# Kernel optimization log

Measured on AMD Instinct MI355X. Metric: run time of the kernel, lower is better.

## Reference

```python
import jax, jax.numpy as jnp
import numpy as np

BS, C, H, W = 16, 192, 120, 120
AN = 36            # agent_num
KS = 3             # kernel_size
POOL = 6           # int(sqrt(agent_num))
MID = 2 * AN // 4  # 18
EPS = 1e-5


def _conv(x, w, groups=1):
    return jax.lax.conv_general_dilated(
        x, w, window_strides=(1, 1), padding='SAME',
        dimension_numbers=('NCHW', 'OIHW', 'NCHW'),
        feature_group_count=groups)


def _bn(x, g, b, m, v):
    # inference-mode BatchNorm2d with running stats
    inv = g / jnp.sqrt(v + EPS)
    return x * inv[None, :, None, None] + (b - m * inv)[None, :, None, None]


def _pool6(x):
    # AdaptiveAvgPool2d(6) with H,W divisible by 6 == exact average pooling
    bs, c, h, w = x.shape
    return x.reshape(bs, c, POOL, h // POOL, POOL, w // POOL).mean(axis=(3, 5))


def setup_inputs() -> dict:
    key = jax.random.key(0)
    ks = jax.random.split(key, 14)
    u = lambda k, s: jax.random.uniform(k, s, jnp.float32, 0.5, 1.5)
    n = lambda k, s, sc: jax.random.normal(k, s, jnp.float32) * sc
    return {
        'x':      n(ks[0], (BS, C, H, W), 1.0),
        'key_w':  n(ks[1], (C, C // 3, KS, KS), 0.05),   # grouped conv, groups=3
        'bn1_g':  u(ks[2], (C,)),
        'bn1_b':  n(ks[3], (C,), 0.1),
        'bn1_m':  n(ks[4], (C,), 0.1),
        'bn1_v':  u(ks[5], (C,)),
        'val_w':  n(ks[6], (C, C, 1, 1), 0.05),
        'att_w1': n(ks[7], (MID, 2 * AN, 1, 1), 0.1),
        'bn2_g':  u(ks[8], (MID,)),
        'bn2_b':  n(ks[9], (MID,), 0.1),
        'bn2_m':  n(ks[10], (MID,), 0.1),
        'bn2_v':  u(ks[11], (MID,)),
        'att_w2': n(ks[12], (KS * KS * AN, MID, 1, 1), 0.1),
        'att_b2': n(ks[13], (KS * KS * AN,), 0.1),
    }


def reference(x, key_w, bn1_g, bn1_b, bn1_m, bn1_v, val_w,
              att_w1, bn2_g, bn2_b, bn2_m, bn2_v, att_w2, att_b2):
    bs, c, h, w = x.shape
    hw = h * w
    # key embedding: grouped conv -> BN -> ReLU
    k1 = jax.nn.relu(_bn(_conv(x, key_w, groups=3), bn1_g, bn1_b, bn1_m, bn1_v))
    # agent tokens and pooled values (torch .view semantics: raw row-major reshape)
    agent = _pool6(x).reshape(bs, AN, c)                 # (bs, 36, c)  channel-mixed view
    v = _pool6(_conv(x, val_w)).reshape(bs, c, AN)       # (bs, c, 36)
    k1r = k1.reshape(bs, hw, c)                          # torch k1.view(bs,-1,c)
    q1 = x.reshape(bs, hw, c)
    # agent<->key and query<->agent attention
    agent_attn = jax.nn.softmax(jnp.einsum('bac,bnc->ban', agent, k1r), axis=-1)  # (bs,36,hw)
    q_attn = jax.nn.softmax(jnp.einsum('bnc,bac->bna', q1, agent), axis=-1)       # (bs,hw,36)
    y = jnp.concatenate([agent_attn, jnp.swapaxes(q_attn, 1, 2)], axis=1)          # (bs,72,hw)
    y = y.reshape(bs, 2 * AN, h, w)
    # conv-generated attention map
    t = jax.nn.relu(_bn(_conv(y, att_w1), bn2_g, bn2_b, bn2_m, bn2_v))
    att = _conv(t, att_w2) + att_b2[None, :, None, None]                           # (bs,324,h,w)
    att = att.reshape(bs, AN, KS * KS, h, w).mean(axis=2).reshape(bs, hw, AN)
    k2 = jax.nn.softmax(att, axis=-1)                                              # (bs,hw,36)
    k2v = jnp.einsum('bna,bca->bnc', k2, v)                                        # (bs,hw,c)
    out = jnp.swapaxes(k2v, 1, 2).reshape(bs, c, h, w) + k1
    return out
```

## Files before the change

kernel.cpp:

```cpp
#include <hip/hip_runtime.h>
#include <hip/hip_bf16.h>
#include <math.h>

#define BS 16
#define C 192
#define H 120
#define W 120
#define HW 14400
#define AN 36
#define MID 18
#define CPG 64
#define EPS 1e-5f
#define SPX 128
#define BPS 200
#define NWQ 13824
#define XROWS 122
#define XCOLS 132
#define OPX 64
#define WST 72

typedef __attribute__((ext_vector_type(8))) short s16x8;
typedef __attribute__((ext_vector_type(4))) float f32x4;
typedef __attribute__((ext_vector_type(4))) unsigned short u16x4;

static __device__ __forceinline__ short f2bf(float f) {
    union { float f; unsigned u; } v; v.f = f;
    unsigned r = (v.u + 0x7FFF + ((v.u >> 16) & 1)) >> 16;
    return (short)r;
}
static __device__ __forceinline__ float bf2f(unsigned short u) {
    union { unsigned u; float f; } v; v.u = ((unsigned)u) << 16;
    return v.f;
}
static __device__ __forceinline__ s16x8 cvt8(float4 f0, float4 f1) {
    s16x8 v;
    v[0] = f2bf(f0.x); v[1] = f2bf(f0.y); v[2] = f2bf(f0.z); v[3] = f2bf(f0.w);
    v[4] = f2bf(f1.x); v[5] = f2bf(f1.y); v[6] = f2bf(f1.z); v[7] = f2bf(f1.w);
    return v;
}

__global__ __launch_bounds__(256) void k_wfold(const float* __restrict__ kw,
                                               const float* __restrict__ g1,
                                               const float* __restrict__ v1,
                                               unsigned short* __restrict__ Wq) {
    int u = blockIdx.x * 256 + threadIdx.x;
    if (u >= NWQ) return;
    int gc = u / 2304, rem = u - gc * 2304;
    int g = gc >> 1, cc = gc & 1;
    int th = rem >> 6, co = rem & 63;
    int tap = th >> 2, hi = th & 3;
    int cog = g * 64 + co;
    float inv = g1[cog] * rsqrtf(v1[cog] + EPS);
    const float* wp = kw + ((size_t)cog * 64 + cc * 32 + hi * 8) * 9 + tap;
    s16x8 v;
    #pragma unroll
    for (int e = 0; e < 8; ++e) v[e] = f2bf(wp[e * 9] * inv);
    *(s16x8*)&Wq[(size_t)u * 8] = v;
}

__global__ __launch_bounds__(256) void k_xt(const float* __restrict__ x,
                                            unsigned short* __restrict__ xTp) {
    int y = blockIdx.x, b = blockIdx.y;
    int t = threadIdx.x;
    __shared__ unsigned short L[120 * 200];
    for (int u = t; u < 24 * 120; u += 256) {
        int oc = u / 120, px = u - oc * 120;
        const float* xp = x + ((size_t)b * C + oc * 8) * HW + y * W + px;
        s16x8 v;
        #pragma unroll
        for (int j = 0; j < 8; ++j) v[j] = f2bf(xp[(size_t)j * HW]);
        *(s16x8*)&L[px * 200 + oc * 8] = v;
    }
    __syncthreads();
    for (int u = t; u < 24 * XCOLS; u += 256) {
        int oc = u / XCOLS, p = u - oc * XCOLS;
        int px = p - 1;
        s16x8 v = {0, 0, 0, 0, 0, 0, 0, 0};
        if (px >= 0 && px < 120) v = *(const s16x8*)&L[px * 200 + oc * 8];
        *(s16x8*)&xTp[(((size_t)(b * 24 + oc)) * XROWS + (y + 1)) * XCOLS * 8 + p * 8] = v;
    }
    if (y == 0 || y == H - 1) {
        int r = (y == 0) ? 0 : XROWS - 1;
        s16x8 z = {0, 0, 0, 0, 0, 0, 0, 0};
        for (int u = t; u < 24 * XCOLS; u += 256) {
            int oc = u / XCOLS, p = u - oc * XCOLS;
            *(s16x8*)&xTp[(((size_t)(b * 24 + oc)) * XROWS + r) * XCOLS * 8 + p * 8] = z;
        }
    }
}

__global__ __launch_bounds__(256) void k_pool_b(const unsigned short* __restrict__ xTp,
                                                float* __restrict__ P) {
    int oc = blockIdx.x, b = blockIdx.y;
    int t = threadIdx.x;
    __shared__ float Lp[240 * 24];
    const unsigned short* base =
        xTp + (((size_t)(b * 24 + oc)) * XROWS + 1) * XCOLS * 8 + 8;
    if (t < 240) {
        int y = t >> 1, h = t & 1;
        const unsigned short* row = base + (size_t)y * XCOLS * 8 + h * 60 * 8;
        float acc[3][8];
        #pragma unroll
        for (int qq = 0; qq < 3; ++qq)
            #pragma unroll
            for (int e = 0; e < 8; ++e) acc[qq][e] = 0.f;
        #pragma unroll
        for (int qq = 0; qq < 3; ++qq)
            for (int j = 0; j < 20; ++j) {
                s16x8 v = *(const s16x8*)&row[(qq * 20 + j) * 8];
                #pragma unroll
                for (int e = 0; e < 8; ++e) acc[qq][e] += bf2f((unsigned short)v[e]);
            }
        #pragma unroll
        for (int qq = 0; qq < 3; ++qq)
            #pragma unroll
            for (int e = 0; e < 8; ++e) Lp[t * 24 + qq * 8 + e] = acc[qq][e];
    }
    __syncthreads();
    if (t < 288) {
        int seg = t >> 3, e = t & 7;
        int yq = seg / 6, q = seg % 6;
        int h = q / 3, qq = q % 3;
        float s = 0.f;
        for (int j = 0; j < 20; ++j)
            s += Lp[((yq * 20 + j) * 2 + h) * 24 + qq * 8 + e];
        P[((size_t)b * C + oc * 8 + e) * AN + seg] = s * (1.f / 400.f);
    }
}

__global__ __launch_bounds__(256) void k_val(const float* __restrict__ valw,
                                             const float* __restrict__ P,
                                             unsigned short* __restrict__ Vb) {
    int b = blockIdx.x;
    __shared__ float Pl[C * AN];
    int tid = threadIdx.x;
    for (int i = tid; i < C * AN; i += 256) Pl[i] = P[(size_t)b * C * AN + i];
    __syncthreads();
    for (int o = tid; o < C * 8; o += 256) {
        int cc = o >> 3, a8 = o & 7;
        s16x8 vv = {0, 0, 0, 0, 0, 0, 0, 0};
        #pragma unroll
        for (int j = 0; j < 8; ++j) {
            int a = a8 * 8 + j;
            if (a < AN) {
                float s = 0.f;
                for (int k = 0; k < C; ++k) s += valw[cc * C + k] * Pl[k * AN + a];
                vv[j] = f2bf(s);
            }
        }
        *(s16x8*)&Vb[((size_t)b * C + cc) * 64 + a8 * 8] = vv;
    }
}

__global__ __launch_bounds__(256, 4) void k_conv_mfma(
        const unsigned short* __restrict__ xTp, const unsigned short* __restrict__ Wq,
        const float* __restrict__ g1, const float* __restrict__ b1,
        const float* __restrict__ m1, const float* __restrict__ v1,
        float* __restrict__ k1f, unsigned short* __restrict__ k1b, int writeF32) {
    int yp = blockIdx.x, g = blockIdx.y, b = blockIdx.z;
    int y0 = yp * 2;
    int t = threadIdx.x;
    __shared__ short xl[(2048 + 2) * 8];

    int w = t >> 6, l = t & 63, lr = l & 15, hi = l >> 4;
    int ry = w >> 1, xh = w & 1;
    f32x4 acc[4][4];
    #pragma unroll
    for (int mt = 0; mt < 4; ++mt)
        #pragma unroll
        for (int nt = 0; nt < 4; ++nt)
            acc[mt][nt] = (f32x4){0.f, 0.f, 0.f, 0.f};

    for (int cc = 0; cc < 2; ++cc) {
        if (cc) __syncthreads();
        const unsigned short* xbase =
            xTp + ((size_t)((b * 24 + g * 8 + cc * 4) * XROWS) + y0) * XCOLS * 8;
        #pragma unroll
        for (int k = 0; k < 8; ++k) {
            int u = t + 256 * k;
            int run = u >> 7, p = u & 127;
            int oct = run >> 2, r = run & 3;
            s16x8 v = *(const s16x8*)&xbase[((size_t)(oct * XROWS + r)) * XCOLS * 8 + p * 8];
            *(s16x8*)&xl[u * 8] = v;
        }
        __syncthreads();
        const s16x8* wq = (const s16x8*)Wq + (size_t)(g * 2 + cc) * 2304;
        s16x8 Bn[4];
        #pragma unroll
        for (int nt = 0; nt < 4; ++nt) Bn[nt] = wq[hi * 64 + nt * 16 + lr];
        #pragma unroll
        for (int tap = 0; tap < 9; ++tap) {
            int ky = tap / 3, kx = tap % 3;
            s16x8 Bc[4];
            #pragma unroll
            for (int nt = 0; nt < 4; ++nt) Bc[nt] = Bn[nt];
            if (tap < 8) {
                #pragma unroll
                for (int nt = 0; nt < 4; ++nt)
                    Bn[nt] = wq[((tap + 1) * 4 + hi) * 64 + nt * 16 + lr];
            }
            s16x8 A[4];
            #pragma unroll
            for (int mt = 0; mt < 4; ++mt) {
                int col = xh * 64 + mt * 16 + lr + kx;
                A[mt] = *(const s16x8*)&xl[((hi * 4 + ry + ky) * 128 + col) * 8];
            }
            #pragma unroll
            for (int mt = 0; mt < 4; ++mt)
                #pragma unroll
                for (int nt = 0; nt < 4; ++nt)
                    acc[mt][nt] = __builtin_amdgcn_mfma_f32_16x16x32_bf16(
                        A[mt], Bc[nt], acc[mt][nt], 0, 0, 0);
        }
    }
    int y = y0 + ry;
    #pragma unroll
    for (int nt = 0; nt < 4; ++nt) {
        int cog = g * CPG + nt * 16 + lr;
        float inv = g1[cog] * rsqrtf(v1[cog] + EPS);
        float beta = b1[cog] - m1[cog] * inv;
        #pragma unroll
        for (int mt = 0; mt < 4; ++mt) {
            int xcol = xh * 64 + mt * 16 + hi * 4;
            if (xcol >= 120) continue;
            float r0 = fmaxf(acc[mt][nt][0] + beta, 0.f);
            float r1 = fmaxf(acc[mt][nt][1] + beta, 0.f);
            float r2 = fmaxf(acc[mt][nt][2] + beta, 0.f);
            float r3 = fmaxf(acc[mt][nt][3] + beta, 0.f);
            size_t base = ((size_t)(b * C + cog)) * HW + y * W + xcol;
            if (writeF32) {
                *(float4*)&k1f[base] = make_float4(r0, r1, r2, r3);
            } else {
                u16x4 q;
                q[0] = (unsigned short)f2bf(r0); q[1] = (unsigned short)f2bf(r1);
                q[2] = (unsigned short)f2bf(r2); q[3] = (unsigned short)f2bf(r3);
                *(u16x4*)&k1b[base] = q;
            }
        }
    }
}

__global__ __launch_bounds__(256, 3) void k_scores_mfma(
        const float* __restrict__ Pp, const float* __restrict__ k1f,
        const unsigned short* __restrict__ k1b, const float* __restrict__ x,
        const unsigned short* __restrict__ xTp,
        float* __restrict__ S1, float* __restrict__ S2) {
    int b = blockIdx.y;
    int n0 = blockIdx.x * SPX;
    int t = threadIdx.x;
    int w = t >> 6, l = t & 63, lr = l & 15, hi = l >> 4;
    __shared__ short Bp[SPX * BPS];

    s16x8 afr[3][6];
    const float* ab = Pp + (size_t)b * (C * AN);
    #pragma unroll
    for (int mt = 0; mt < 3; ++mt) {
        int row = mt * 16 + lr;
        #pragma unroll
        for (int kc = 0; kc < 6; ++kc) {
            s16x8 v = {0, 0, 0, 0, 0, 0, 0, 0};
            if (row < AN) {
                const float4* ap = (const float4*)(ab + row * C + kc * 32 + hi * 8);
                v = cvt8(ap[0], ap[1]);
            }
            afr[mt][kc] = v;
        }
    }

    #pragma unroll 1
    for (int s = 0; s < 2; ++s) {
        __syncthreads();
        if (s == 0 && k1b) {
            const unsigned short* src = k1b + (size_t)b * C * HW + (size_t)n0 * C;
            for (int i = t; i < SPX * 24; i += 256) {
                int row = i / 24, o = i - row * 24;
                s16x8 v = {0, 0, 0, 0, 0, 0, 0, 0};
                if (n0 + row < HW) v = *(const s16x8*)&src[row * C + o * 8];
                *(s16x8*)&Bp[row * BPS + o * 8] = v;
            }
        } else if (s == 1 && xTp) {
            for (int i = t; i < SPX * 24; i += 256) {
                int row = i / 24, oc = i - row * 24;
                int n = n0 + row;
                s16x8 v = {0, 0, 0, 0, 0, 0, 0, 0};
                if (n < HW) {
                    int yy = n / 120, xx = n - yy * 120;
                    v = *(const s16x8*)&xTp[(((size_t)(b * 24 + oc)) * XROWS + yy + 1) *
                                            XCOLS * 8 + (xx + 1) * 8];
                }
                *(s16x8*)&Bp[row * BPS + oc * 8] = v;
            }
        } else {
            const float* sf = (s == 0) ? k1f : x;
            const float4* src = (const float4*)(sf + (size_t)b * C * HW + (size_t)n0 * C);
            for (int i = t; i < SPX * 24; i += 256) {
                int row = i / 24, c8 = (i - row * 24) * 8;
                s16x8 v = {0, 0, 0, 0, 0, 0, 0, 0};
                if (n0 + row < HW)
                    v = cvt8(src[row * 48 + c8 / 4], src[row * 48 + c8 / 4 + 1]);
                *(s16x8*)&Bp[row * BPS + c8] = v;
            }
        }
        __syncthreads();
        f32x4 acc[3][2];
        #pragma unroll
        for (int mt = 0; mt < 3; ++mt)
            #pragma unroll
            for (int pt = 0; pt < 2; ++pt)
                acc[mt][pt] = (f32x4){0.f, 0.f, 0.f, 0.f};
        #pragma unroll
        for (int kc = 0; kc < 6; ++kc) {
            s16x8 bf[2];
            #pragma unroll
            for (int pt = 0; pt < 2; ++pt) {
                int px = (w * 2 + pt) * 16 + lr;
                bf[pt] = *(const s16x8*)&Bp[px * BPS + kc * 32 + hi * 8];
            }
            #pragma unroll
            for (int mt = 0; mt < 3; ++mt)
                #pragma unroll
                for (int pt = 0; pt < 2; ++pt)
                    acc[mt][pt] = __builtin_amdgcn_mfma_f32_16x16x32_bf16(
                        afr[mt][kc], bf[pt], acc[mt][pt], 0, 0, 0);
        }
        float* dst = (s == 0 ? S1 : S2) + (size_t)b * AN * HW + n0;
        #pragma unroll
        for (int mt = 0; mt < 3; ++mt)
            #pragma unroll
            for (int pt = 0; pt < 2; ++pt) {
                int px = (w * 2 + pt) * 16 + lr;
                if (n0 + px >= HW) continue;
                #pragma unroll
                for (int r = 0; r < 4; ++r) {
                    int a = mt * 16 + hi * 4 + r;
                    if (a < AN) dst[(size_t)a * HW + px] = acc[mt][pt][r];
                }
            }
    }
}

__global__ __launch_bounds__(256) void k_rowstats(const float* __restrict__ S,
                                                  float* __restrict__ stats) {
    int row = blockIdx.x;
    const float* p = S + (size_t)row * HW;
    int tid = threadIdx.x;
    __shared__ float red[4];
    float m = -1e30f;
    for (int i = tid; i < HW / 4; i += 256) {
        float4 v = ((const float4*)p)[i];
        m = fmaxf(m, fmaxf(fmaxf(v.x, v.y), fmaxf(v.z, v.w)));
    }
    #pragma unroll
    for (int off = 32; off > 0; off >>= 1) m = fmaxf(m, __shfl_down(m, off, 64));
    if ((tid & 63) == 0) red[tid >> 6] = m;
    __syncthreads();
    m = fmaxf(fmaxf(red[0], red[1]), fmaxf(red[2], red[3]));
    __syncthreads();
    float s = 0.f;
    for (int i = tid; i < HW / 4; i += 256) {
        float4 v = ((const float4*)p)[i];
        s += __expf(v.x - m) + __expf(v.y - m) + __expf(v.z - m) + __expf(v.w - m);
    }
    #pragma unroll
    for (int off = 32; off > 0; off >>= 1) s += __shfl_down(s, off, 64);
    if ((tid & 63) == 0) red[tid >> 6] = s;
    __syncthreads();
    if (tid == 0) {
        stats[row] = m;
        stats[576 + row] = 1.f / (red[0] + red[1] + red[2] + red[3]);
    }
}

__global__ __launch_bounds__(256) void k_fuse(const float* __restrict__ A1,
                                              const float* __restrict__ stats,
                                              const float* __restrict__ S2,
                                              const float* __restrict__ w1,
                                              const float* __restrict__ g2,
                                              const float* __restrict__ b2,
                                              const float* __restrict__ m2,
                                              const float* __restrict__ v2,
                                              const float* __restrict__ w2,
                                              const float* __restrict__ bias2,
                                              unsigned short* __restrict__ AMb) {
    int b = blockIdx.y;
    int tid = threadIdx.x;
    int N = blockIdx.x * 256 + tid;
    __shared__ float W1f[MID * 72];
    __shared__ float b1f[MID];
    __shared__ float W2m[AN * MID];
    __shared__ float b2m[AN];
    __shared__ float sm_m[AN], sm_ri[AN];
    for (int i = tid; i < MID * 72; i += 256) {
        int m = i / 72;
        W1f[i] = w1[i] * (g2[m] * rsqrtf(v2[m] + EPS));
    }
    if (tid < MID) {
        float inv = g2[tid] * rsqrtf(v2[tid] + EPS);
        b1f[tid] = b2[tid] - m2[tid] * inv;
    }
    for (int i = tid; i < AN * MID; i += 256) {
        int a = i / MID, m = i % MID;
        float s = 0.f;
        #pragma unroll
        for (int k = 0; k < 9; ++k) s += w2[(a * 9 + k) * MID + m];
        W2m[i] = s * (1.f / 9.f);
    }
    if (tid < AN) {
        float s = 0.f;
        #pragma unroll
        for (int k = 0; k < 9; ++k) s += bias2[tid * 9 + k];
        b2m[tid] = s * (1.f / 9.f);
        sm_m[tid] = stats[b * AN + tid];
        sm_ri[tid] = stats[576 + b * AN + tid];
    }
    __syncthreads();
    if (N >= HW) return;
    float yv[72];
    const float* a1p = A1 + (size_t)b * AN * HW + N;
    #pragma unroll
    for (int j = 0; j < AN; ++j)
        yv[j] = __expf(a1p[(size_t)j * HW] - sm_m[j]) * sm_ri[j];
    const float* s2p = S2 + (size_t)b * AN * HW + N;
    float mx = -1e30f;
    #pragma unroll
    for (int j = 0; j < AN; ++j) {
        float v = s2p[(size_t)j * HW];
        yv[AN + j] = v;
        mx = fmaxf(mx, v);
    }
    float ssum = 0.f;
    #pragma unroll
    for (int j = 0; j < AN; ++j) {
        float e = __expf(yv[AN + j] - mx);
        yv[AN + j] = e;
        ssum += e;
    }
    float rs = 1.f / ssum;
    #pragma unroll
    for (int j = 0; j < AN; ++j) yv[AN + j] *= rs;
    float t[MID];
    #pragma unroll
    for (int m = 0; m < MID; ++m) {
        float a = b1f[m];
        #pragma unroll
        for (int j = 0; j < 72; ++j) a += W1f[m * 72 + j] * yv[j];
        t[m] = a > 0.f ? a : 0.f;
    }
    unsigned short* amp = AMb + (size_t)b * AN * HW + N;
    #pragma unroll
    for (int a = 0; a < AN; ++a) {
        float acc = b2m[a];
        #pragma unroll
        for (int m = 0; m < MID; ++m) acc += W2m[a * MID + m] * t[m];
        amp[(size_t)a * HW] = (unsigned short)f2bf(acc);
    }
}

__global__ __launch_bounds__(256) void k_out_mfma(const unsigned short* __restrict__ AMb,
                                                  const unsigned short* __restrict__ Vb,
                                                  const unsigned short* __restrict__ k1b,
                                                  float* __restrict__ outp) {
    int b = blockIdx.y;
    int N0 = blockIdx.x * OPX;
    int t = threadIdx.x;
    __shared__ float smemf[4 * 1088];
    short* wl = (short*)smemf;

    {
        int p = t >> 2, q = t & 3;
        int N = N0 + p;
        int a = N / 400;
        int n0w = (N - a * 400) * AN;
        const unsigned short* amp = AMb + ((size_t)b * AN + a) * HW + n0w;
        const int qoff = (q == 0) ? 0 : (q == 1) ? 12 : (q == 2) ? 20 : 32;
        const int qn4 = (q == 0) ? 3 : (q == 1) ? 2 : (q == 2) ? 3 : 1;
        float vals[12];
        const u16x4* ap = (const u16x4*)(amp + qoff);
        #pragma unroll
        for (int i = 0; i < 3; ++i) {
            if (i < qn4) {
                u16x4 v = ap[i];
                vals[i * 4 + 0] = bf2f(v[0]); vals[i * 4 + 1] = bf2f(v[1]);
                vals[i * 4 + 2] = bf2f(v[2]); vals[i * 4 + 3] = bf2f(v[3]);
            }
        }
        int cnt = qn4 * 4;
        float m = -1e30f;
        #pragma unroll
        for (int i = 0; i < 12; ++i) if (i < cnt) m = fmaxf(m, vals[i]);
        m = fmaxf(m, __shfl_xor(m, 1, 64));
        m = fmaxf(m, __shfl_xor(m, 2, 64));
        float s = 0.f;
        #pragma unroll
        for (int i = 0; i < 12; ++i)
            if (i < cnt) { vals[i] = __expf(vals[i] - m); s += vals[i]; }
        s += __shfl_xor(s, 1, 64);
        s += __shfl_xor(s, 2, 64);
        float rs = 1.f / s;
        #pragma unroll
        for (int i = 0; i < 12; ++i)
            if (i < cnt) wl[p * WST + qoff + i] = f2bf(vals[i] * rs);
        if (q == 3) {
            #pragma unroll
            for (int i = 36; i < 64; ++i) wl[p * WST + i] = 0;
        }
    }
    __syncthreads();

    int w = t >> 6, l = t & 63, lr = l & 15, hi = l >> 4;
    int cc0 = w * 48;
    const s16x8* vb = (const s16x8*)(Vb + (size_t)b * C * 64);
    s16x8 Af[3][2];
    #pragma unroll
    for (int mt = 0; mt < 3; ++mt)
        #pragma unroll
        for (int ch = 0; ch < 2; ++ch)
            Af[mt][ch] = vb[(cc0 + mt * 16 + lr) * 8 + ch * 4 + hi];
    f32x4 acc[3][4];
    #pragma unroll
    for (int mt = 0; mt < 3; ++mt)
        #pragma unroll
        for (int pt = 0; pt < 4; ++pt)
            acc[mt][pt] = (f32x4){0.f, 0.f, 0.f, 0.f};
    #pragma unroll
    for (int pt = 0; pt < 4; ++pt) {
        s16x8 Bf[2];
        #pragma unroll
        for (int ch = 0; ch < 2; ++ch)
            Bf[ch] = *(const s16x8*)&wl[(pt * 16 + lr) * WST + ch * 32 + hi * 8];
        #pragma unroll
        for (int ch = 0; ch < 2; ++ch)
            #pragma unroll
            for (int mt = 0; mt < 3; ++mt)
                acc[mt][pt] = __builtin_amdgcn_mfma_f32_16x16x32_bf16(
                    Af[mt][ch], Bf[ch], acc[mt][pt], 0, 0, 0);
    }
    __syncthreads();

    float* T = smemf + (size_t)w * 1088;
    #pragma unroll
    for (int mt = 0; mt < 3; ++mt) {
        #pragma unroll
        for (int pt = 0; pt < 4; ++pt)
            #pragma unroll
            for (int r = 0; r < 4; ++r)
                T[(hi * 4 + r) * 68 + pt * 16 + lr] = acc[mt][pt][r];
        #pragma unroll
        for (int pass = 0; pass < 4; ++pass) {
            int ccr = pass * 4 + hi;
            int px4 = (l & 15) * 4;
            float4 vv = *(float4*)&T[ccr * 68 + px4];
            int cc = cc0 + mt * 16 + ccr;
            size_t idx = ((size_t)(b * C + cc)) * HW + N0 + px4;
            float4 res;
            if (k1b) {
                u16x4 kk = *(const u16x4*)&k1b[idx];
                res = make_float4(bf2f(kk[0]), bf2f(kk[1]), bf2f(kk[2]), bf2f(kk[3]));
            } else {
                res = *(float4*)&outp[idx];
            }
            vv.x += res.x; vv.y += res.y; vv.z += res.z; vv.w += res.w;
            *(float4*)&outp[idx] = vv;
        }
    }
}

extern "C" void kernel_launch(void* const* d_in, const int* in_sizes, int n_in,
                              void* d_out, int out_size, void* d_ws, size_t ws_size,
                              hipStream_t stream) {
    const float* x      = (const float*)d_in[0];
    const float* key_w  = (const float*)d_in[1];
    const float* bn1_g  = (const float*)d_in[2];
    const float* bn1_b  = (const float*)d_in[3];
    const float* bn1_m  = (const float*)d_in[4];
    const float* bn1_v  = (const float*)d_in[5];
    const float* val_w  = (const float*)d_in[6];
    const float* att_w1 = (const float*)d_in[7];
    const float* bn2_g  = (const float*)d_in[8];
    const float* bn2_b  = (const float*)d_in[9];
    const float* bn2_m  = (const float*)d_in[10];
    const float* bn2_v  = (const float*)d_in[11];
    const float* att_w2 = (const float*)d_in[12];
    const float* att_b2 = (const float*)d_in[13];
    float* out = (float*)d_out;

    unsigned char* base = (unsigned char*)d_ws;
    size_t off = 0;
    unsigned short* Wq = (unsigned short*)(base + off); off += 221184;
    unsigned short* Vb = (unsigned short*)(base + off); off += 393216;
    float* P  = (float*)(base + off); off += 442368;
    float* ST = (float*)(base + off); off += 4608;
    float* S1 = (float*)(base + off); off += 33177600;
    float* S2 = (float*)(base + off); off += 33177600;
    unsigned short* AMb = (unsigned short*)(base + off); off += 33177600;
    size_t k1bBytes = (size_t)BS * C * HW * 2;
    size_t xtpBytes = (size_t)BS * 24 * XROWS * XCOLS * 16;
    unsigned short* k1b = nullptr;
    unsigned short* xTp = (unsigned short*)S1;
    int xtpSep = 0;
    if (ws_size >= off + k1bBytes) {
        k1b = (unsigned short*)(base + off); off += k1bBytes;
        if (ws_size >= off + xtpBytes) {
            xTp = (unsigned short*)(base + off); off += xtpBytes;
            xtpSep = 1;
        }
    }
    int writeF32 = (k1b == nullptr) ? 1 : 0;

    k_wfold<<<(NWQ + 255) / 256, 256, 0, stream>>>(key_w, bn1_g, bn1_v, Wq);
    k_xt<<<dim3(H, BS), 256, 0, stream>>>(x, xTp);
    k_pool_b<<<dim3(24, BS), 256, 0, stream>>>(xTp, P);
    k_val<<<BS, 256, 0, stream>>>(val_w, P, Vb);
    k_conv_mfma<<<dim3(H / 2, 3, BS), 256, 0, stream>>>(
        xTp, Wq, bn1_g, bn1_b, bn1_m, bn1_v, out, k1b, writeF32);
    k_scores_mfma<<<dim3((HW + SPX - 1) / SPX, BS), 256, 0, stream>>>(
        P, out, k1b, x, xtpSep ? xTp : nullptr, S1, S2);
    k_rowstats<<<BS * AN, 256, 0, stream>>>(S1, ST);
    k_fuse<<<dim3((HW + 255) / 256, BS), 256, 0, stream>>>(
        S1, ST, S2, att_w1, bn2_g, bn2_b, bn2_m, bn2_v, att_w2, att_b2, AMb);
    k_out_mfma<<<dim3(HW / OPX, BS), 256, 0, stream>>>(AMb, Vb, k1b, out);
}
```

Baseline: 457.0 us.

## Fuse softmax stats into scores kernel and store scores as bf16

The scores kernel now computes per-block online-softmax partials (max, sum) for the agent-attention rows and a full per-pixel softmax for the query-attention scores, writing both score tensors as bf16 instead of fp32. A small reduction kernel merges the per-block partials, replacing the full-row stats pass over the fp32 score tensor, and the fuse kernel reads bf16 inputs without recomputing the query softmax. This removes a large read pass and halves intermediate traffic, at the cost of bf16 rounding of logits before exponentiation and a reshuffled workspace layout that aliases xTp.

```diff
diff --git a/kernel.cpp b/kernel.cpp
--- a/kernel.cpp
+++ b/kernel.cpp
@@ -18,6 +18,7 @@
 #define XCOLS 132
 #define OPX 64
 #define WST 72
+#define NBLK 113
 
 typedef __attribute__((ext_vector_type(8))) short s16x8;
 typedef __attribute__((ext_vector_type(4))) float f32x4;
@@ -244,12 +245,15 @@
         const float* __restrict__ Pp, const float* __restrict__ k1f,
         const unsigned short* __restrict__ k1b, const float* __restrict__ x,
         const unsigned short* __restrict__ xTp,
-        float* __restrict__ S1, float* __restrict__ S2) {
+        unsigned short* __restrict__ S1b, unsigned short* __restrict__ S2n,
+        float2* __restrict__ PS) {
     int b = blockIdx.y;
-    int n0 = blockIdx.x * SPX;
+    int bx = blockIdx.x;
+    int n0 = bx * SPX;
     int t = threadIdx.x;
     int w = t >> 6, l = t & 63, lr = l & 15, hi = l >> 4;
     __shared__ short Bp[SPX * BPS];
+    __shared__ float2 Ls[4][40];
 
     s16x8 afr[3][6];
     const float* ab = Pp + (size_t)b * (C * AN);
@@ -323,57 +327,130 @@
                     acc[mt][pt] = __builtin_amdgcn_mfma_f32_16x16x32_bf16(
                         afr[mt][kc], bf[pt], acc[mt][pt], 0, 0, 0);
         }
-        float* dst = (s == 0 ? S1 : S2) + (size_t)b * AN * HW + n0;
-        #pragma unroll
-        for (int mt = 0; mt < 3; ++mt)
+        if (s == 0) {
+            unsigned short* dst = S1b + (size_t)b * AN * HW + n0;
+            #pragma unroll
+            for (int mt = 0; mt < 3; ++mt)
+                #pragma unroll
+                for (int pt = 0; pt < 2; ++pt) {
+                    int px = (w * 2 + pt) * 16 + lr;
+                    if (n0 + px >= HW) continue;
+                    #pragma unroll
+                    for (int r = 0; r < 4; ++r) {
+                        int a = mt * 16 + hi * 4 + r;
+                        if (a < AN)
+                            dst[(size_t)a * HW + px] = (unsigned short)f2bf(acc[mt][pt][r]);
+                    }
+                }
+            bool ok0 = (n0 + (w * 2) * 16 + lr) < HW;
+            bool ok1 = (n0 + (w * 2 + 1) * 16 + lr) < HW;
+            #pragma unroll
+            for (int mt = 0; mt < 3; ++mt)
+                #pragma unroll
+                for (int r = 0; r < 4; ++r) {
+                    float v0 = ok0 ? acc[mt][0][r] : -1e30f;
+                    float v1 = ok1 ? acc[mt][1][r] : -1e30f;
+                    float m = fmaxf(v0, v1);
+                    #pragma unroll
+                    for (int mk = 1; mk <= 8; mk <<= 1)
+                        m = fmaxf(m, __shfl_xor(m, mk, 64));
+                    float e = (ok0 ? __expf(v0 - m) : 0.f) + (ok1 ? __expf(v1 - m) : 0.f);
+                    #pragma unroll
+                    for (int mk = 1; mk <= 8; mk <<= 1)
+                        e += __shfl_xor(e, mk, 64);
+                    int a = mt * 16 + hi * 4 + r;
+                    if (lr == 0 && a < AN) Ls[w][a] = make_float2(m, e);
+                }
+        } else {
+            unsigned short* dst = S2n + (size_t)b * AN * HW + n0;
             #pragma unroll
             for (int pt = 0; pt < 2; ++pt) {
                 int px = (w * 2 + pt) * 16 + lr;
-                if (n0 + px >= HW) continue;
-                #pragma unroll
-                for (int r = 0; r < 4; ++r) {
-                    int a = mt * 16 + hi * 4 + r;
-                    if (a < AN) dst[(size_t)a * HW + px] = acc[mt][pt][r];
+                float pmax = -1e30f;
+                #pragma unroll
+                for (int mt = 0; mt < 3; ++mt)
+                    #pragma unroll
+                    for (int r = 0; r < 4; ++r) {
+                        int a = mt * 16 + hi * 4 + r;
+                        if (a < AN) pmax = fmaxf(pmax, acc[mt][pt][r]);
+                    }
+                pmax = fmaxf(pmax, __shfl_xor(pmax, 16, 64));
+                pmax = fmaxf(pmax, __shfl_xor(pmax, 32, 64));
+                float psum = 0.f;
+                #pragma unroll
+                for (int mt = 0; mt < 3; ++mt)
+                    #pragma unroll
+                    for (int r = 0; r < 4; ++r) {
+                        int a = mt * 16 + hi * 4 + r;
+                        float e = (a < AN) ? __expf(acc[mt][pt][r] - pmax) : 0.f;
+                        acc[mt][pt][r] = e;
+                        psum += e;
+                    }
+                psum += __shfl_xor(psum, 16, 64);
+                psum += __shfl_xor(psum, 32, 64);
+                float rs = 1.f / psum;
+                if (n0 + px < HW) {
+                    #pragma unroll
+                    for (int mt = 0; mt < 3; ++mt)
+                        #pragma unroll
+                        for (int r = 0; r < 4; ++r) {
+                            int a = mt * 16 + hi * 4 + r;
+                            if (a < AN)
+                                dst[(size_t)a * HW + px] =
+                                    (unsigned short)f2bf(acc[mt][pt][r] * rs);
+                        }
                 }
             }
-    }
-}
-
-__global__ __launch_bounds__(256) void k_rowstats(const float* __restrict__ S,
+        }
+    }
+    __syncthreads();
+    if (t < AN) {
+        float m = -1e30f, ssum = 0.f;
+        #pragma unroll
+        for (int wv = 0; wv < 4; ++wv) {
+            float2 p = Ls[wv][t];
+            float mn = fmaxf(m, p.x);
+            ssum = ssum * __expf(m - mn) + p.y * __expf(p.x - mn);
+            m = mn;
+        }
+        PS[((size_t)b * AN + t) * NBLK + bx] = make_float2(m, ssum);
+    }
+}
+
+__global__ __launch_bounds__(128) void k_redstats(const float2* __restrict__ PS,
                                                   float* __restrict__ stats) {
     int row = blockIdx.x;
-    const float* p = S + (size_t)row * HW;
-    int tid = threadIdx.x;
-    __shared__ float red[4];
-    float m = -1e30f;
-    for (int i = tid; i < HW / 4; i += 256) {
-        float4 v = ((const float4*)p)[i];
-        m = fmaxf(m, fmaxf(fmaxf(v.x, v.y), fmaxf(v.z, v.w)));
-    }
-    #pragma unroll
-    for (int off = 32; off > 0; off >>= 1) m = fmaxf(m, __shfl_down(m, off, 64));
-    if ((tid & 63) == 0) red[tid >> 6] = m;
-    __syncthreads();
-    m = fmaxf(fmaxf(red[0], red[1]), fmaxf(red[2], red[3]));
-    __syncthreads();
-    float s = 0.f;
-    for (int i = tid; i < HW / 4; i += 256) {
-        float4 v = ((const float4*)p)[i];
-        s += __expf(v.x - m) + __expf(v.y - m) + __expf(v.z - m) + __expf(v.w - m);
-    }
-    #pragma unroll
-    for (int off = 32; off > 0; off >>= 1) s += __shfl_down(s, off, 64);
-    if ((tid & 63) == 0) red[tid >> 6] = s;
-    __syncthreads();
-    if (tid == 0) {
-        stats[row] = m;
-        stats[576 + row] = 1.f / (red[0] + red[1] + red[2] + red[3]);
-    }
-}
-
-__global__ __launch_bounds__(256) void k_fuse(const float* __restrict__ A1,
+    int t = threadIdx.x;
+    float m = -1e30f, s = 0.f;
+    for (int i = t; i < NBLK; i += 128) {
+        float2 p = PS[(size_t)row * NBLK + i];
+        float mn = fmaxf(m, p.x);
+        s = s * __expf(m - mn) + p.y * __expf(p.x - mn);
+        m = mn;
+    }
+    #pragma unroll
+    for (int off = 32; off > 0; off >>= 1) {
+        float om = __shfl_down(m, off, 64);
+        float os = __shfl_down(s, off, 64);
+        float mn = fmaxf(m, om);
+        s = s * __expf(m - mn) + os * __expf(om - mn);
+        m = mn;
+    }
+    __shared__ float2 red[2];
+    if ((t & 63) == 0) red[t >> 6] = make_float2(m, s);
+    __syncthreads();
+    if (t == 0) {
+        float2 a = red[0], bb = red[1];
+        float mn = fmaxf(a.x, bb.x);
+        float ss = a.y * __expf(a.x - mn) + bb.y * __expf(bb.x - mn);
+        stats[row] = mn;
+        stats[576 + row] = 1.f / ss;
+    }
+}
+
+__global__ __launch_bounds__(256) void k_fuse(const unsigned short* __restrict__ S1b,
                                               const float* __restrict__ stats,
-                                              const float* __restrict__ S2,
+                                              const unsigned short* __restrict__ S2n,
                                               const float* __restrict__ w1,
                                               const float* __restrict__ g2,
                                               const float* __restrict__ b2,
@@ -416,28 +493,13 @@
     __syncthreads();
     if (N >= HW) return;
     float yv[72];
-    const float* a1p = A1 + (size_t)b * AN * HW + N;
+    const unsigned short* a1p = S1b + (size_t)b * AN * HW + N;
     #pragma unroll
     for (int j = 0; j < AN; ++j)
-        yv[j] = __expf(a1p[(size_t)j * HW] - sm_m[j]) * sm_ri[j];
-    const float* s2p = S2 + (size_t)b * AN * HW + N;
-    float mx = -1e30f;
-    #pragma unroll
-    for (int j = 0; j < AN; ++j) {
-        float v = s2p[(size_t)j * HW];
-        yv[AN + j] = v;
-        mx = fmaxf(mx, v);
-    }
-    float ssum = 0.f;
-    #pragma unroll
-    for (int j = 0; j < AN; ++j) {
-        float e = __expf(yv[AN + j] - mx);
-        yv[AN + j] = e;
-        ssum += e;
-    }
-    float rs = 1.f / ssum;
-    #pragma unroll
-    for (int j = 0; j < AN; ++j) yv[AN + j] *= rs;
+        yv[j] = __expf(bf2f(a1p[(size_t)j * HW]) - sm_m[j]) * sm_ri[j];
+    const unsigned short* s2p = S2n + (size_t)b * AN * HW + N;
+    #pragma unroll
+    for (int j = 0; j < AN; ++j) yv[AN + j] = bf2f(s2p[(size_t)j * HW]);
     float t[MID];
     #pragma unroll
     for (int m = 0; m < MID; ++m) {
@@ -590,13 +652,17 @@
     unsigned short* Vb = (unsigned short*)(base + off); off += 393216;
     float* P  = (float*)(base + off); off += 442368;
     float* ST = (float*)(base + off); off += 4608;
-    float* S1 = (float*)(base + off); off += 33177600;
-    float* S2 = (float*)(base + off); off += 33177600;
-    unsigned short* AMb = (unsigned short*)(base + off); off += 33177600;
+    float2* PS = (float2*)(base + off); off += 520704;
+    unsigned char* big = base + off;
+    size_t nS2 = (size_t)BS * AN * HW * 2;
+    size_t xtpBytes = (size_t)BS * 24 * XROWS * XCOLS * 16;
+    unsigned short* S1b = (unsigned short*)big;
+    unsigned short* S2n = (unsigned short*)(big + nS2);
+    unsigned short* AMb = (unsigned short*)(big + 2 * nS2);
+    off += xtpBytes;
     size_t k1bBytes = (size_t)BS * C * HW * 2;
-    size_t xtpBytes = (size_t)BS * 24 * XROWS * XCOLS * 16;
     unsigned short* k1b = nullptr;
-    unsigned short* xTp = (unsigned short*)S1;
+    unsigned short* xTp = (unsigned short*)big;
     int xtpSep = 0;
     if (ws_size >= off + k1bBytes) {
         k1b = (unsigned short*)(base + off); off += k1bBytes;
@@ -613,10 +679,10 @@
     k_val<<<BS, 256, 0, stream>>>(val_w, P, Vb);
     k_conv_mfma<<<dim3(H / 2, 3, BS), 256, 0, stream>>>(
         xTp, Wq, bn1_g, bn1_b, bn1_m, bn1_v, out, k1b, writeF32);
-    k_scores_mfma<<<dim3((HW + SPX - 1) / SPX, BS), 256, 0, stream>>>(
-        P, out, k1b, x, xtpSep ? xTp : nullptr, S1, S2);
-    k_rowstats<<<BS * AN, 256, 0, stream>>>(S1, ST);
+    k_scores_mfma<<<dim3(NBLK, BS), 256, 0, stream>>>(
+        P, out, k1b, x, xtpSep ? xTp : nullptr, S1b, S2n, PS);
+    k_redstats<<<BS * AN, 128, 0, stream>>>(PS, ST);
     k_fuse<<<dim3((HW + 255) / 256, BS), 256, 0, stream>>>(
-        S1, ST, S2, att_w1, bn2_g, bn2_b, bn2_m, bn2_v, att_w2, att_b2, AMb);
+        S1b, ST, S2n, att_w1, bn2_g, bn2_b, bn2_m, bn2_v, att_w2, att_b2, AMb);
     k_out_mfma<<<dim3(HW / OPX, BS), 256, 0, stream>>>(AMb, Vb, k1b, out);
 }
```

Result: slower. 468.1 us (+2.4%).
